# Optimization experiments

Hardware: AMD Instinct MI355X
Metric: run time of the kernel (lower is better)

The kernel has to match this reference:

```python
import jax, jax.numpy as jnp
import numpy as np
from jax import lax

B, C, HID, H, W = 8, 256, 64, 64, 64

def conv3x3(x, w, b):
    # x: [B,C_in,H,W], w: [C_out,C_in,3,3], b: [C_out]
    y = lax.conv_general_dilated(x, w, window_strides=(1, 1), padding='SAME',
                                 dimension_numbers=('NCHW', 'OIHW', 'NCHW'))
    return y + b[None, :, None, None]

def setup_inputs() -> dict:
    key = jax.random.key(0)
    ks = jax.random.split(key, 7)
    s_in = 1.0 / np.sqrt(C * 9)
    return {
        'x': jax.random.normal(ks[0], (B, C, H, W), dtype=jnp.float32),
        'Wq': jax.random.normal(ks[1], (HID, C, 3, 3), dtype=jnp.float32) * s_in,
        'bq': jax.random.normal(ks[2], (HID,), dtype=jnp.float32) * s_in,
        'Wk': jax.random.normal(ks[3], (HID, C, 3, 3), dtype=jnp.float32) * s_in,
        'bk': jax.random.normal(ks[4], (HID,), dtype=jnp.float32) * s_in,
        'Wv': jax.random.normal(ks[5], (C, C, 3, 3), dtype=jnp.float32) * s_in,
        'bv': jax.random.normal(ks[6], (C,), dtype=jnp.float32) * s_in,
    }

def reference(x, Wq, bq, Wk, bk, Wv, bv):
    b, c, w, h = x.shape
    n = w * h
    q = conv3x3(x, Wq, bq).reshape(b, -1, n).transpose(0, 2, 1)  # [B,N,hid]
    k = conv3x3(x, Wk, bk).reshape(b, -1, n)                      # [B,hid,N]
    v = conv3x3(x, Wv, bv).reshape(b, c, n)                       # [B,C,N]
    attn = jax.nn.softmax(jnp.einsum('bnd,bdm->bnm', q, k), axis=-1)  # [B,N,N]
    # out = bmm(value, attn^T): out[b,c,m] = sum_n v[b,c,n] * attn[b,m,n]
    out = jnp.einsum('bcn,bmn->bcm', v, attn).reshape(b, c, w, h)
    # F.interpolate(out, h, mode='bilinear') with H==W is an exact identity
    return out + x
```

## Files before the change

### kernel.cpp

```cpp
#include <hip/hip_runtime.h>
#include <math.h>

#define NB   8
#define NC   256
#define ND   64
#define NPIX 4096

typedef short bf16x8 __attribute__((ext_vector_type(8)));
typedef float f32x4  __attribute__((ext_vector_type(4)));
typedef float f32x16 __attribute__((ext_vector_type(16)));

static __device__ __forceinline__ ushort f2bf(float f) {
    uint u = __float_as_uint(f);
    u += 0x7fffu + ((u >> 16) & 1u);
    return (ushort)(u >> 16);
}
static __device__ __forceinline__ float bf2f(ushort h) {
    return __uint_as_float(((uint)h) << 16);
}

__global__ __launch_bounds__(256) void prep_k(
    const float* __restrict__ x,
    const float* __restrict__ Wq, const float* __restrict__ Wk,
    const float* __restrict__ Wv,
    ushort* __restrict__ xth, ushort* __restrict__ xtl,
    ushort* __restrict__ qh, ushort* __restrict__ ql,
    ushort* __restrict__ kh, ushort* __restrict__ kl,
    ushort* __restrict__ vh)
{
    __shared__ char shbuf[64 * 68 * 4];
    const int id = blockIdx.x;
    const int t = threadIdx.x;

    if (id < 384) {
        float* wb = (float*)shbuf;
        const int g = id;
        const float* src;
        ushort *dh, *dl;
        int co, Co, split;
        if (g < 64)       { src = Wq + (size_t)g * 2304; co = g;       Co = 64;  dh = qh; dl = ql; split = 1; }
        else if (g < 128) { src = Wk + (size_t)(g - 64) * 2304; co = g - 64; Co = 64; dh = kh; dl = kl; split = 1; }
        else              { src = Wv + (size_t)(g - 128) * 2304; co = g - 128; Co = 256; dh = vh; dl = nullptr; split = 0; }

        for (int i = t; i < 2304; i += 256) wb[i] = src[i];
        __syncthreads();
        for (int j = t; j < 2304; j += 256) {
            const int rs = j >> 8, ci = j & 255;
            const float v = wb[ci * 9 + rs];
            const ushort hv = f2bf(v);
            const size_t o = ((size_t)(rs * Co + co)) * 256 + ci;
            dh[o] = hv;
            if (split) dl[o] = f2bf(v - bf2f(hv));
        }
    } else {
        float (*tile)[68] = (float(*)[68])shbuf;
        const int xid = id - 384;
        const int b = xid & 7;
        const int p0 = ((xid >> 3) & 63) * 64;
        const int c0 = (xid >> 9) * 64;

        const int cl = t >> 4, p4 = (t & 15) * 4;
        #pragma unroll
        for (int i = 0; i < 4; i++) {
            const int c = cl + 16 * i;
            *(float4*)&tile[c][p4] =
                *(const float4*)&x[((size_t)(b * NC + c0 + c)) * NPIX + p0 + p4];
        }
        __syncthreads();

        const int pl = t & 63, ch = t >> 6;
        float v[16];
        #pragma unroll
        for (int j = 0; j < 16; j++) v[j] = tile[ch * 16 + j][pl];
        ushort h[16], l[16];
        #pragma unroll
        for (int j = 0; j < 16; j++) {
            h[j] = f2bf(v[j]);
            l[j] = f2bf(v[j] - bf2f(h[j]));
        }
        const size_t o = ((size_t)(b * NPIX + p0 + pl)) * 256 + c0 + ch * 16;
        *(uint4*)&xth[o]     = *(uint4*)&h[0];
        *(uint4*)&xth[o + 8] = *(uint4*)&h[8];
        *(uint4*)&xtl[o]     = *(uint4*)&l[0];
        *(uint4*)&xtl[o + 8] = *(uint4*)&l[8];
    }
}

__global__ __launch_bounds__(256) void conv_split_k(
    const ushort* __restrict__ xth, const ushort* __restrict__ xtl,
    const ushort* __restrict__ wqh, const ushort* __restrict__ wql,
    const ushort* __restrict__ wkh, const ushort* __restrict__ wkl,
    const float* __restrict__ bq, const float* __restrict__ bk,
    ushort* __restrict__ qoh, ushort* __restrict__ qol,
    ushort* __restrict__ koh, ushort* __restrict__ kol)
{
    extern __shared__ char smem[];
    ushort* xsh = (ushort*)smem;
    ushort* xsl = xsh + 6 * 66 * 24;
    ushort* wsp = xsl + 6 * 66 * 24;
    float*  sbias = (float*)(wsp + 9 * 64 * 24);

    const int id = blockIdx.x;
    const int b = id & 7, hq = (id >> 3) & 15, ct = id >> 7;
    const ushort* wth = ct ? wkh : wqh;
    const ushort* wtl = ct ? wkl : wql;
    const float*  bias = ct ? bk : bq;
    ushort* outh = ct ? koh : qoh;
    ushort* outl = ct ? kol : qol;

    const int t = threadIdx.x;
    const int wv = t >> 6, lane = t & 63;
    const int l31 = lane & 31, khl = lane >> 5;
    const int lanebase = l31 * 24 + khl * 8;
    const int h = hq * 4 + wv;

    if (t < 64) sbias[t] = bias[t];
    for (int i = t; i < 384; i += 256) {
        const int p = i / 192, r2 = i % 192;
        const int row = r2 / 32, e = (r2 % 32) / 16, ci = r2 & 15;
        (p ? xsl : xsh)[(row * 66 + e * 65) * 24 + ci] = 0;
    }

    f32x16 a00 = {0}, a01 = {0}, a10 = {0}, a11 = {0};

    for (int ch = 0; ch < 16; ch++) {
        __syncthreads();
        const int ci0 = ch * 16;
        #pragma unroll
        for (int pl2 = 0; pl2 < 2; pl2++) {
            const ushort* src = pl2 ? xtl : xth;
            ushort* dst = pl2 ? xsl : xsh;
            #pragma unroll
            for (int i = 0; i < 3; i++) {
                const int a = i * 256 + t;
                const int cih = a & 1, col = (a >> 1) & 63, row = a >> 7;
                const int hs = hq * 4 + row - 1;
                uint4 val = {0, 0, 0, 0};
                if (hs >= 0 && hs < 64)
                    val = *(const uint4*)&src[((size_t)(b * NPIX + hs * 64 + col)) * 256 + ci0 + cih * 8];
                *(uint4*)&dst[(row * 66 + 1 + col) * 24 + cih * 8] = val;
            }
        }
        #pragma unroll
        for (int i = 0; i < 5; i++) {
            const int a = i * 256 + t;
            if (a < 1152) {
                const int cih = a & 1, co = (a >> 1) & 63, rs = a >> 7;
                uint4 wv4 = *(const uint4*)&wth[((size_t)(rs * 64 + co)) * 256 + ci0 + cih * 8];
                *(uint4*)&wsp[(rs * 64 + co) * 24 + cih * 8] = wv4;
            }
        }
        __syncthreads();
        #pragma unroll
        for (int rs = 0; rs < 9; rs++) {
            const int r = rs / 3, s = rs % 3;
            bf16x8 A0 = *(const bf16x8*)&wsp[rs * 1536 + lanebase];
            bf16x8 A1 = *(const bf16x8*)&wsp[rs * 1536 + 768 + lanebase];
            const int xo = ((wv + r) * 66 + s) * 24 + lanebase;
            bf16x8 B0h = *(const bf16x8*)&xsh[xo];
            bf16x8 B1h = *(const bf16x8*)&xsh[xo + 768];
            bf16x8 B0l = *(const bf16x8*)&xsl[xo];
            bf16x8 B1l = *(const bf16x8*)&xsl[xo + 768];
            a00 = __builtin_amdgcn_mfma_f32_32x32x16_bf16(A0, B0h, a00, 0, 0, 0);
            a01 = __builtin_amdgcn_mfma_f32_32x32x16_bf16(A0, B1h, a01, 0, 0, 0);
            a10 = __builtin_amdgcn_mfma_f32_32x32x16_bf16(A1, B0h, a10, 0, 0, 0);
            a11 = __builtin_amdgcn_mfma_f32_32x32x16_bf16(A1, B1h, a11, 0, 0, 0);
            a00 = __builtin_amdgcn_mfma_f32_32x32x16_bf16(A0, B0l, a00, 0, 0, 0);
            a01 = __builtin_amdgcn_mfma_f32_32x32x16_bf16(A0, B1l, a01, 0, 0, 0);
            a10 = __builtin_amdgcn_mfma_f32_32x32x16_bf16(A1, B0l, a10, 0, 0, 0);
            a11 = __builtin_amdgcn_mfma_f32_32x32x16_bf16(A1, B1l, a11, 0, 0, 0);
        }
        __syncthreads();
        #pragma unroll
        for (int i = 0; i < 5; i++) {
            const int a = i * 256 + t;
            if (a < 1152) {
                const int cih = a & 1, co = (a >> 1) & 63, rs = a >> 7;
                uint4 wv4 = *(const uint4*)&wtl[((size_t)(rs * 64 + co)) * 256 + ci0 + cih * 8];
                *(uint4*)&wsp[(rs * 64 + co) * 24 + cih * 8] = wv4;
            }
        }
        __syncthreads();
        #pragma unroll
        for (int rs = 0; rs < 9; rs++) {
            const int r = rs / 3, s = rs % 3;
            bf16x8 A0 = *(const bf16x8*)&wsp[rs * 1536 + lanebase];
            bf16x8 A1 = *(const bf16x8*)&wsp[rs * 1536 + 768 + lanebase];
            const int xo = ((wv + r) * 66 + s) * 24 + lanebase;
            bf16x8 B0h = *(const bf16x8*)&xsh[xo];
            bf16x8 B1h = *(const bf16x8*)&xsh[xo + 768];
            a00 = __builtin_amdgcn_mfma_f32_32x32x16_bf16(A0, B0h, a00, 0, 0, 0);
            a01 = __builtin_amdgcn_mfma_f32_32x32x16_bf16(A0, B1h, a01, 0, 0, 0);
            a10 = __builtin_amdgcn_mfma_f32_32x32x16_bf16(A1, B0h, a10, 0, 0, 0);
            a11 = __builtin_amdgcn_mfma_f32_32x32x16_bf16(A1, B1h, a11, 0, 0, 0);
        }
    }

    const float4* sb4 = (const float4*)sbias;
    #pragma unroll
    for (int ms = 0; ms < 2; ms++)
        #pragma unroll
        for (int ns = 0; ns < 2; ns++) {
            const f32x16 av = ms ? (ns ? a11 : a10) : (ns ? a01 : a00);
            const int p = h * 64 + ns * 32 + l31;
            #pragma unroll
            for (int g = 0; g < 4; g++) {
                const float4 bi = sb4[ms * 8 + 2 * g + khl];
                float v0 = av[4 * g + 0] + bi.x;
                float v1 = av[4 * g + 1] + bi.y;
                float v2 = av[4 * g + 2] + bi.z;
                float v3 = av[4 * g + 3] + bi.w;
                ushort4 hv, lv;
                hv.x = f2bf(v0); lv.x = f2bf(v0 - bf2f(hv.x));
                hv.y = f2bf(v1); lv.y = f2bf(v1 - bf2f(hv.y));
                hv.z = f2bf(v2); lv.z = f2bf(v2 - bf2f(hv.z));
                hv.w = f2bf(v3); lv.w = f2bf(v3 - bf2f(hv.w));
                const size_t o = ((size_t)(b * NPIX + p)) * 64 + ms * 32 + 8 * g + 4 * khl;
                *(ushort4*)&outh[o] = hv;
                *(ushort4*)&outl[o] = lv;
            }
        }
}

__global__ __launch_bounds__(256) void conv_v_k(
    const ushort* __restrict__ xth, const ushort* __restrict__ wtv,
    const float* __restrict__ bv, ushort* __restrict__ vout)
{
    extern __shared__ char smem[];
    ushort* xsh = (ushort*)smem;
    ushort* wsp = xsh + 6 * 66 * 24;
    float*  sbias = (float*)(wsp + 9 * 64 * 24);

    const int id = blockIdx.x;
    const int b = id & 7, hq = (id >> 3) & 15, co0 = (id >> 7) * 64;
    const int t = threadIdx.x;
    const int wv = t >> 6, lane = t & 63;
    const int l31 = lane & 31, khl = lane >> 5;
    const int lanebase = l31 * 24 + khl * 8;
    const int h = hq * 4 + wv;

    if (t < 64) sbias[t] = bv[co0 + t];
    for (int i = t; i < 192; i += 256) {
        const int row = i / 32, e = (i % 32) / 16, ci = i & 15;
        xsh[(row * 66 + e * 65) * 24 + ci] = 0;
    }

    f32x16 a00 = {0}, a01 = {0}, a10 = {0}, a11 = {0};

    for (int ch = 0; ch < 16; ch++) {
        __syncthreads();
        const int ci0 = ch * 16;
        #pragma unroll
        for (int i = 0; i < 3; i++) {
            const int a = i * 256 + t;
            const int cih = a & 1, col = (a >> 1) & 63, row = a >> 7;
            const int hs = hq * 4 + row - 1;
            uint4 val = {0, 0, 0, 0};
            if (hs >= 0 && hs < 64)
                val = *(const uint4*)&xth[((size_t)(b * NPIX + hs * 64 + col)) * 256 + ci0 + cih * 8];
            *(uint4*)&xsh[(row * 66 + 1 + col) * 24 + cih * 8] = val;
        }
        #pragma unroll
        for (int i = 0; i < 5; i++) {
            const int a = i * 256 + t;
            if (a < 1152) {
                const int cih = a & 1, co = (a >> 1) & 63, rs = a >> 7;
                uint4 wv4 = *(const uint4*)&wtv[((size_t)(rs * 256 + co0 + co)) * 256 + ci0 + cih * 8];
                *(uint4*)&wsp[(rs * 64 + co) * 24 + cih * 8] = wv4;
            }
        }
        __syncthreads();
        #pragma unroll
        for (int rs = 0; rs < 9; rs++) {
            const int r = rs / 3, s = rs % 3;
            const int xo = ((wv + r) * 66 + s) * 24 + lanebase;
            bf16x8 A0 = *(const bf16x8*)&xsh[xo];
            bf16x8 A1 = *(const bf16x8*)&xsh[xo + 768];
            bf16x8 B0 = *(const bf16x8*)&wsp[rs * 1536 + lanebase];
            bf16x8 B1 = *(const bf16x8*)&wsp[rs * 1536 + 768 + lanebase];
            a00 = __builtin_amdgcn_mfma_f32_32x32x16_bf16(A0, B0, a00, 0, 0, 0);
            a01 = __builtin_amdgcn_mfma_f32_32x32x16_bf16(A0, B1, a01, 0, 0, 0);
            a10 = __builtin_amdgcn_mfma_f32_32x32x16_bf16(A1, B0, a10, 0, 0, 0);
            a11 = __builtin_amdgcn_mfma_f32_32x32x16_bf16(A1, B1, a11, 0, 0, 0);
        }
    }

    #pragma unroll
    for (int ns = 0; ns < 2; ns++) {
        const int co = co0 + ns * 32 + l31;
        const float bi = sbias[ns * 32 + l31];
        #pragma unroll
        for (int ms = 0; ms < 2; ms++) {
            const f32x16 av = ms ? (ns ? a11 : a10) : (ns ? a01 : a00);
            #pragma unroll
            for (int g = 0; g < 4; g++) {
                const int p = h * 64 + ms * 32 + 8 * g + 4 * khl;
                ushort4 ov;
                ov.x = f2bf(av[4 * g + 0] + bi);
                ov.y = f2bf(av[4 * g + 1] + bi);
                ov.z = f2bf(av[4 * g + 2] + bi);
                ov.w = f2bf(av[4 * g + 3] + bi);
                *(ushort4*)&vout[((size_t)(b * NC + co)) * NPIX + p] = ov;
            }
        }
    }
}

__global__ __launch_bounds__(256, 2) void attn_k(
    const ushort* __restrict__ qh, const ushort* __restrict__ ql,
    const ushort* __restrict__ kh, const ushort* __restrict__ kl,
    const ushort* __restrict__ vb, const float* __restrict__ x,
    float* __restrict__ out)
{
    const int id = blockIdx.x;
    const int b  = id & 7;
    const int m0 = (id >> 3) * 64;
    const int t  = threadIdx.x;
    const int w  = t >> 6;
    const int lane = t & 63;
    const int quad = lane >> 4;
    const int l16  = lane & 15;

    __shared__ ushort sps[2][64 * 64];
    __shared__ float  red[4][64];
    __shared__ float  ivl[64];

    bf16x8 aqh[4][2], aql[4][2];
    #pragma unroll
    for (int mg = 0; mg < 4; mg++)
        #pragma unroll
        for (int ks = 0; ks < 2; ks++) {
            const size_t g = ((size_t)b * NPIX + m0 + mg * 16 + l16) * ND + ks * 32 + quad * 8;
            aqh[mg][ks] = *(const bf16x8*)&qh[g];
            aql[mg][ks] = *(const bf16x8*)&ql[g];
        }

    const size_t kbase = ((size_t)b * NPIX + 16 * w + l16) * ND + quad * 8;
    size_t vbase[4];
    #pragma unroll
    for (int ct = 0; ct < 4; ct++)
        vbase[ct] = ((size_t)b * NC + 64 * w + ct * 16 + l16) * NPIX + quad * 8;

    bf16x8 kfh[2], kfl[2], vf[4][2];
    #pragma unroll
    for (int ks = 0; ks < 2; ks++) {
        kfh[ks] = *(const bf16x8*)&kh[kbase + ks * 32];
        kfl[ks] = *(const bf16x8*)&kl[kbase + ks * 32];
    }
    #pragma unroll
    for (int ct = 0; ct < 4; ct++)
        #pragma unroll
        for (int ks = 0; ks < 2; ks++)
            vf[ct][ks] = *(const bf16x8*)&vb[vbase[ct] + ks * 32];

    f32x4 acc[4][4];
    #pragma unroll
    for (int i = 0; i < 4; i++)
        #pragma unroll
        for (int j = 0; j < 4; j++) acc[i][j] = (f32x4){0.f, 0.f, 0.f, 0.f};
    float lsum[4] = {0.f, 0.f, 0.f, 0.f};

    auto qk_tile = [&](int obuf) {
        #pragma unroll
        for (int mg = 0; mg < 4; mg++) {
            f32x4 s = {0.f, 0.f, 0.f, 0.f};
            #pragma unroll
            for (int ks = 0; ks < 2; ks++) {
                s = __builtin_amdgcn_mfma_f32_16x16x32_bf16(kfh[ks], aqh[mg][ks], s, 0, 0, 0);
                s = __builtin_amdgcn_mfma_f32_16x16x32_bf16(kfl[ks], aqh[mg][ks], s, 0, 0, 0);
                s = __builtin_amdgcn_mfma_f32_16x16x32_bf16(kfh[ks], aql[mg][ks], s, 0, 0, 0);
            }
            const ushort p0 = f2bf(__expf(s[0] - 30.f));
            const ushort p1 = f2bf(__expf(s[1] - 30.f));
            const ushort p2 = f2bf(__expf(s[2] - 30.f));
            const ushort p3 = f2bf(__expf(s[3] - 30.f));
            lsum[mg] += (bf2f(p0) + bf2f(p1)) + (bf2f(p2) + bf2f(p3));
            uint2 pk;
            pk.x = (uint)p0 | ((uint)p1 << 16);
            pk.y = (uint)p2 | ((uint)p3 << 16);
            const int row = mg * 16 + l16;
            const int bo = (32 * w + quad * 8) ^ ((row & 7) << 4);
            *(uint2*)((char*)&sps[obuf][0] + row * 128 + bo) = pk;
        }
    };

    qk_tile(0);
    {
        const size_t kb = kbase + (size_t)64 * ND;
        #pragma unroll
        for (int ks = 0; ks < 2; ks++) {
            kfh[ks] = *(const bf16x8*)&kh[kb + ks * 32];
            kfl[ks] = *(const bf16x8*)&kl[kb + ks * 32];
        }
    }
    asm volatile("s_waitcnt lgkmcnt(0)\n\ts_barrier" ::: "memory");

    for (int n0 = 0; n0 < NPIX; n0 += 64) {
        const int buf = (n0 >> 6) & 1;
        const bool nxt = (n0 + 64) < NPIX;

        bf16x8 ap[2][4];
        #pragma unroll
        for (int ks = 0; ks < 2; ks++)
            #pragma unroll
            for (int mg = 0; mg < 4; mg++) {
                const int row = mg * 16 + l16;
                const int bo = (ks * 64 + quad * 16) ^ ((row & 7) << 4);
                ap[ks][mg] = *(const bf16x8*)((const char*)&sps[buf][0] + row * 128 + bo);
            }

        if (nxt) qk_tile(buf ^ 1);

        #pragma unroll
        for (int ks = 0; ks < 2; ks++)
            #pragma unroll
            for (int mg = 0; mg < 4; mg++)
                #pragma unroll
                for (int ct = 0; ct < 4; ct++)
                    acc[mg][ct] = __builtin_amdgcn_mfma_f32_16x16x32_bf16(
                        ap[ks][mg], vf[ct][ks], acc[mg][ct], 0, 0, 0);

        if (n0 + 128 < NPIX) {
            const size_t kb = kbase + (size_t)(n0 + 128) * ND;
            #pragma unroll
            for (int ks = 0; ks < 2; ks++) {
                kfh[ks] = *(const bf16x8*)&kh[kb + ks * 32];
                kfl[ks] = *(const bf16x8*)&kl[kb + ks * 32];
            }
        }
        if (nxt) {
            #pragma unroll
            for (int ct = 0; ct < 4; ct++)
                #pragma unroll
                for (int ks = 0; ks < 2; ks++)
                    vf[ct][ks] = *(const bf16x8*)&vb[vbase[ct] + n0 + 64 + ks * 32];
        }

        asm volatile("s_waitcnt lgkmcnt(0)\n\ts_barrier" ::: "memory");
    }

    #pragma unroll
    for (int mg = 0; mg < 4; mg++) {
        lsum[mg] += __shfl_xor(lsum[mg], 16, 64);
        lsum[mg] += __shfl_xor(lsum[mg], 32, 64);
    }
    if (quad == 0) {
        #pragma unroll
        for (int mg = 0; mg < 4; mg++) red[w][mg * 16 + l16] = lsum[mg];
    }
    __syncthreads();
    if (t < 64)
        ivl[t] = 1.f / (red[0][t] + red[1][t] + red[2][t] + red[3][t]);
    __syncthreads();

    #pragma unroll
    for (int mg = 0; mg < 4; mg++) {
        const int mrow = mg * 16 + quad * 4;
        const float4 il4 = *(const float4*)&ivl[mrow];
        const int m = m0 + mrow;
        #pragma unroll
        for (int ct = 0; ct < 4; ct++) {
            const int c = 64 * w + ct * 16 + l16;
            const size_t base = ((size_t)b * NC + c) * NPIX + m;
            const float4 xv = *(const float4*)&x[base];
            const f32x4 a = acc[mg][ct];
            float4 o;
            o.x = fmaf(a[0], il4.x, xv.x);
            o.y = fmaf(a[1], il4.y, xv.y);
            o.z = fmaf(a[2], il4.z, xv.z);
            o.w = fmaf(a[3], il4.w, xv.w);
            *(float4*)&out[base] = o;
        }
    }
}

extern "C" void kernel_launch(void* const* d_in, const int* in_sizes, int n_in,
                              void* d_out, int out_size, void* d_ws, size_t ws_size,
                              hipStream_t stream)
{
    const float* x  = (const float*)d_in[0];
    const float* Wq = (const float*)d_in[1];
    const float* bq = (const float*)d_in[2];
    const float* Wk = (const float*)d_in[3];
    const float* bk = (const float*)d_in[4];
    const float* Wv = (const float*)d_in[5];
    const float* bv = (const float*)d_in[6];
    float* outp = (float*)d_out;

    const size_t XT = (size_t)NB * NPIX * 256;
    const size_t QK = (size_t)NB * NPIX * ND;
    ushort* xt_h = (ushort*)d_ws;
    ushort* xt_l = xt_h + XT;
    ushort* v_b  = xt_l;
    ushort* q_h  = xt_l + XT;
    ushort* q_l  = q_h + QK;
    ushort* k_h  = q_l + QK;
    ushort* k_l  = k_h + QK;
    ushort* wtq_h = k_l + QK;
    ushort* wtq_l = wtq_h + 147456;
    ushort* wtk_h = wtq_l + 147456;
    ushort* wtk_l = wtk_h + 147456;
    ushort* wtv_h = wtk_l + 147456;

    dim3 blk(256);
    prep_k<<<dim3(2432), blk, 0, stream>>>(
        x, Wq, Wk, Wv, xt_h, xt_l, wtq_h, wtq_l, wtk_h, wtk_l, wtv_h);
    conv_split_k<<<dim3(256), blk, 65920, stream>>>(
        xt_h, xt_l, wtq_h, wtq_l, wtk_h, wtk_l, bq, bk, q_h, q_l, k_h, k_l);
    conv_v_k<<<dim3(512), blk, 46912, stream>>>(xt_h, wtv_h, bv, v_b);
    attn_k<<<dim3(512), blk, 0, stream>>>(q_h, q_l, k_h, k_l, v_b, x, outp);
}
```

Measured before the change: 419.6 us.

## Load conv weight fragments directly into registers instead of staging in LDS

```diff
diff --git a/kernel.cpp b/kernel.cpp
--- a/kernel.cpp
+++ b/kernel.cpp
@@ -86,7 +86,7 @@
     }
 }
 
-__global__ __launch_bounds__(256) void conv_split_k(
+__global__ __launch_bounds__(256, 1) void conv_split_k(
     const ushort* __restrict__ xth, const ushort* __restrict__ xtl,
     const ushort* __restrict__ wqh, const ushort* __restrict__ wql,
     const ushort* __restrict__ wkh, const ushort* __restrict__ wkl,
@@ -97,8 +97,7 @@
     extern __shared__ char smem[];
     ushort* xsh = (ushort*)smem;
     ushort* xsl = xsh + 6 * 66 * 24;
-    ushort* wsp = xsl + 6 * 66 * 24;
-    float*  sbias = (float*)(wsp + 9 * 64 * 24);
+    float*  sbias = (float*)(xsl + 6 * 66 * 24);
 
     const int id = blockIdx.x;
     const int b = id & 7, hq = (id >> 3) & 15, ct = id >> 7;
@@ -121,11 +120,24 @@
         (p ? xsl : xsh)[(row * 66 + e * 65) * 24 + ci] = 0;
     }
 
+    const size_t wbase = (size_t)l31 * 256 + khl * 8;
+
     f32x16 a00 = {0}, a01 = {0}, a10 = {0}, a11 = {0};
 
     for (int ch = 0; ch < 16; ch++) {
+        const int ci0 = ch * 16;
+
+        bf16x8 whA0[9], whA1[9], wlA0[9], wlA1[9];
+        #pragma unroll
+        for (int rs = 0; rs < 9; rs++) {
+            const size_t o = (size_t)rs * 16384 + wbase + ci0;
+            whA0[rs] = *(const bf16x8*)&wth[o];
+            whA1[rs] = *(const bf16x8*)&wth[o + 8192];
+            wlA0[rs] = *(const bf16x8*)&wtl[o];
+            wlA1[rs] = *(const bf16x8*)&wtl[o + 8192];
+        }
+
         __syncthreads();
-        const int ci0 = ch * 16;
         #pragma unroll
         for (int pl2 = 0; pl2 < 2; pl2++) {
             const ushort* src = pl2 ? xtl : xth;
@@ -141,58 +153,35 @@
                 *(uint4*)&dst[(row * 66 + 1 + col) * 24 + cih * 8] = val;
             }
         }
-        #pragma unroll
-        for (int i = 0; i < 5; i++) {
-            const int a = i * 256 + t;
-            if (a < 1152) {
-                const int cih = a & 1, co = (a >> 1) & 63, rs = a >> 7;
-                uint4 wv4 = *(const uint4*)&wth[((size_t)(rs * 64 + co)) * 256 + ci0 + cih * 8];
-                *(uint4*)&wsp[(rs * 64 + co) * 24 + cih * 8] = wv4;
-            }
-        }
         __syncthreads();
+
         #pragma unroll
         for (int rs = 0; rs < 9; rs++) {
             const int r = rs / 3, s = rs % 3;
-            bf16x8 A0 = *(const bf16x8*)&wsp[rs * 1536 + lanebase];
-            bf16x8 A1 = *(const bf16x8*)&wsp[rs * 1536 + 768 + lanebase];
             const int xo = ((wv + r) * 66 + s) * 24 + lanebase;
             bf16x8 B0h = *(const bf16x8*)&xsh[xo];
             bf16x8 B1h = *(const bf16x8*)&xsh[xo + 768];
             bf16x8 B0l = *(const bf16x8*)&xsl[xo];
             bf16x8 B1l = *(const bf16x8*)&xsl[xo + 768];
-            a00 = __builtin_amdgcn_mfma_f32_32x32x16_bf16(A0, B0h, a00, 0, 0, 0);
-            a01 = __builtin_amdgcn_mfma_f32_32x32x16_bf16(A0, B1h, a01, 0, 0, 0);
-            a10 = __builtin_amdgcn_mfma_f32_32x32x16_bf16(A1, B0h, a10, 0, 0, 0);
-            a11 = __builtin_amdgcn_mfma_f32_32x32x16_bf16(A1, B1h, a11, 0, 0, 0);
-            a00 = __builtin_amdgcn_mfma_f32_32x32x16_bf16(A0, B0l, a00, 0, 0, 0);
-            a01 = __builtin_amdgcn_mfma_f32_32x32x16_bf16(A0, B1l, a01, 0, 0, 0);
-            a10 = __builtin_amdgcn_mfma_f32_32x32x16_bf16(A1, B0l, a10, 0, 0, 0);
-            a11 = __builtin_amdgcn_mfma_f32_32x32x16_bf16(A1, B1l, a11, 0, 0, 0);
-        }
-        __syncthreads();
-        #pragma unroll
-        for (int i = 0; i < 5; i++) {
-            const int a = i * 256 + t;
-            if (a < 1152) {
-                const int cih = a & 1, co = (a >> 1) & 63, rs = a >> 7;
-                uint4 wv4 = *(const uint4*)&wtl[((size_t)(rs * 64 + co)) * 256 + ci0 + cih * 8];
-                *(uint4*)&wsp[(rs * 64 + co) * 24 + cih * 8] = wv4;
-            }
-        }
-        __syncthreads();
+            a00 = __builtin_amdgcn_mfma_f32_32x32x16_bf16(whA0[rs], B0h, a00, 0, 0, 0);
+            a01 = __builtin_amdgcn_mfma_f32_32x32x16_bf16(whA0[rs], B1h, a01, 0, 0, 0);
+            a10 = __builtin_amdgcn_mfma_f32_32x32x16_bf16(whA1[rs], B0h, a10, 0, 0, 0);
+            a11 = __builtin_amdgcn_mfma_f32_32x32x16_bf16(whA1[rs], B1h, a11, 0, 0, 0);
+            a00 = __builtin_amdgcn_mfma_f32_32x32x16_bf16(whA0[rs], B0l, a00, 0, 0, 0);
+            a01 = __builtin_amdgcn_mfma_f32_32x32x16_bf16(whA0[rs], B1l, a01, 0, 0, 0);
+            a10 = __builtin_amdgcn_mfma_f32_32x32x16_bf16(whA1[rs], B0l, a10, 0, 0, 0);
+            a11 = __builtin_amdgcn_mfma_f32_32x32x16_bf16(whA1[rs], B1l, a11, 0, 0, 0);
+        }
         #pragma unroll
         for (int rs = 0; rs < 9; rs++) {
             const int r = rs / 3, s = rs % 3;
-            bf16x8 A0 = *(const bf16x8*)&wsp[rs * 1536 + lanebase];
-            bf16x8 A1 = *(const bf16x8*)&wsp[rs * 1536 + 768 + lanebase];
             const int xo = ((wv + r) * 66 + s) * 24 + lanebase;
             bf16x8 B0h = *(const bf16x8*)&xsh[xo];
             bf16x8 B1h = *(const bf16x8*)&xsh[xo + 768];
-            a00 = __builtin_amdgcn_mfma_f32_32x32x16_bf16(A0, B0h, a00, 0, 0, 0);
-            a01 = __builtin_amdgcn_mfma_f32_32x32x16_bf16(A0, B1h, a01, 0, 0, 0);
-            a10 = __builtin_amdgcn_mfma_f32_32x32x16_bf16(A1, B0h, a10, 0, 0, 0);
-            a11 = __builtin_amdgcn_mfma_f32_32x32x16_bf16(A1, B1h, a11, 0, 0, 0);
+            a00 = __builtin_amdgcn_mfma_f32_32x32x16_bf16(wlA0[rs], B0h, a00, 0, 0, 0);
+            a01 = __builtin_amdgcn_mfma_f32_32x32x16_bf16(wlA0[rs], B1h, a01, 0, 0, 0);
+            a10 = __builtin_amdgcn_mfma_f32_32x32x16_bf16(wlA1[rs], B0h, a10, 0, 0, 0);
+            a11 = __builtin_amdgcn_mfma_f32_32x32x16_bf16(wlA1[rs], B1h, a11, 0, 0, 0);
         }
     }
 
@@ -222,14 +211,13 @@
         }
 }
 
-__global__ __launch_bounds__(256) void conv_v_k(
+__global__ __launch_bounds__(256, 2) void conv_v_k(
     const ushort* __restrict__ xth, const ushort* __restrict__ wtv,
     const float* __restrict__ bv, ushort* __restrict__ vout)
 {
     extern __shared__ char smem[];
     ushort* xsh = (ushort*)smem;
-    ushort* wsp = xsh + 6 * 66 * 24;
-    float*  sbias = (float*)(wsp + 9 * 64 * 24);
+    float*  sbias = (float*)(xsh + 6 * 66 * 24);
 
     const int id = blockIdx.x;
     const int b = id & 7, hq = (id >> 3) & 15, co0 = (id >> 7) * 64;
@@ -245,11 +233,22 @@
         xsh[(row * 66 + e * 65) * 24 + ci] = 0;
     }
 
+    const size_t wbase = (size_t)(co0 + l31) * 256 + khl * 8;
+
     f32x16 a00 = {0}, a01 = {0}, a10 = {0}, a11 = {0};
 
     for (int ch = 0; ch < 16; ch++) {
+        const int ci0 = ch * 16;
+
+        bf16x8 wB0[9], wB1[9];
+        #pragma unroll
+        for (int rs = 0; rs < 9; rs++) {
+            const size_t o = (size_t)rs * 65536 + wbase + ci0;
+            wB0[rs] = *(const bf16x8*)&wtv[o];
+            wB1[rs] = *(const bf16x8*)&wtv[o + 8192];
+        }
+
         __syncthreads();
-        const int ci0 = ch * 16;
         #pragma unroll
         for (int i = 0; i < 3; i++) {
             const int a = i * 256 + t;
@@ -260,28 +259,18 @@
                 val = *(const uint4*)&xth[((size_t)(b * NPIX + hs * 64 + col)) * 256 + ci0 + cih * 8];
             *(uint4*)&xsh[(row * 66 + 1 + col) * 24 + cih * 8] = val;
         }
-        #pragma unroll
-        for (int i = 0; i < 5; i++) {
-            const int a = i * 256 + t;
-            if (a < 1152) {
-                const int cih = a & 1, co = (a >> 1) & 63, rs = a >> 7;
-                uint4 wv4 = *(const uint4*)&wtv[((size_t)(rs * 256 + co0 + co)) * 256 + ci0 + cih * 8];
-                *(uint4*)&wsp[(rs * 64 + co) * 24 + cih * 8] = wv4;
-            }
-        }
         __syncthreads();
+
         #pragma unroll
         for (int rs = 0; rs < 9; rs++) {
             const int r = rs / 3, s = rs % 3;
             const int xo = ((wv + r) * 66 + s) * 24 + lanebase;
             bf16x8 A0 = *(const bf16x8*)&xsh[xo];
             bf16x8 A1 = *(const bf16x8*)&xsh[xo + 768];
-            bf16x8 B0 = *(const bf16x8*)&wsp[rs * 1536 + lanebase];
-            bf16x8 B1 = *(const bf16x8*)&wsp[rs * 1536 + 768 + lanebase];
-            a00 = __builtin_amdgcn_mfma_f32_32x32x16_bf16(A0, B0, a00, 0, 0, 0);
-            a01 = __builtin_amdgcn_mfma_f32_32x32x16_bf16(A0, B1, a01, 0, 0, 0);
-            a10 = __builtin_amdgcn_mfma_f32_32x32x16_bf16(A1, B0, a10, 0, 0, 0);
-            a11 = __builtin_amdgcn_mfma_f32_32x32x16_bf16(A1, B1, a11, 0, 0, 0);
+            a00 = __builtin_amdgcn_mfma_f32_32x32x16_bf16(A0, wB0[rs], a00, 0, 0, 0);
+            a01 = __builtin_amdgcn_mfma_f32_32x32x16_bf16(A0, wB1[rs], a01, 0, 0, 0);
+            a10 = __builtin_amdgcn_mfma_f32_32x32x16_bf16(A1, wB0[rs], a10, 0, 0, 0);
+            a11 = __builtin_amdgcn_mfma_f32_32x32x16_bf16(A1, wB1[rs], a11, 0, 0, 0);
         }
     }
 
@@ -505,8 +494,8 @@
     dim3 blk(256);
     prep_k<<<dim3(2432), blk, 0, stream>>>(
         x, Wq, Wk, Wv, xt_h, xt_l, wtq_h, wtq_l, wtk_h, wtk_l, wtv_h);
-    conv_split_k<<<dim3(256), blk, 65920, stream>>>(
+    conv_split_k<<<dim3(256), blk, 38272, stream>>>(
         xt_h, xt_l, wtq_h, wtq_l, wtk_h, wtk_l, bq, bk, q_h, q_l, k_h, k_l);
-    conv_v_k<<<dim3(512), blk, 46912, stream>>>(xt_h, wtv_h, bv, v_b);
+    conv_v_k<<<dim3(512), blk, 19264, stream>>>(xt_h, wtv_h, bv, v_b);
     attn_k<<<dim3(512), blk, 0, stream>>>(q_h, q_l, k_h, k_l, v_b, x, outp);
 }
```

Result: slower. 499.6 us (+19.1%).
